# Kernel optimization log

Measured on AMD Instinct MI355X. Metric: run time of the kernel, lower is better.

The kernel has to match this reference:

```python
import jax, jax.numpy as jnp
import numpy as np

B, C_IN, C_OUT, H, W, K, NK = 16, 256, 256, 64, 64, 3, 2
EPS = 1e-8


def setup_inputs() -> dict:
    key = jax.random.key(0)
    k1, k2, k3, k4 = jax.random.split(key, 4)
    x = jax.random.normal(k1, (B, C_IN, H, W), dtype=jnp.float32)
    mod = jax.random.normal(k2, (B, C_IN), dtype=jnp.float32)
    kernel_mod = jax.random.normal(k3, (B, NK), dtype=jnp.float32)
    # kernel bank: [num_conv_kernels, dim_out, dim_in, k, k] (kaiming-ish scale)
    weights = jax.random.normal(k4, (NK, C_OUT, C_IN, K, K), dtype=jnp.float32) / np.sqrt(C_IN * K * K)
    gamma = jnp.ones((C_OUT,), dtype=jnp.float32)
    return {"x": x, "mod": mod, "kernel_mod": kernel_mod, "weights": weights, "gamma": gamma}


def _block(x, mod, kernel_mod, weights, gamma):
    # adaptive kernel selection: softmax-mix the kernel bank per sample
    attn = jax.nn.softmax(kernel_mod, axis=-1)                       # [b, n]
    w = jnp.einsum('bn,noikl->boikl', attn, weights)                 # [b, o, i, k, k]
    # style modulation over input channels
    w = w * (mod[:, None, :, None, None] + 1.0)
    # demodulation
    denom = jnp.clip(jnp.sum(w * w, axis=(2, 3, 4), keepdims=True), EPS)
    w = w * jax.lax.rsqrt(denom)
    # per-sample conv (groups=b trick in torch) -> vmap over batch
    def conv_one(fmap, wb):
        return jax.lax.conv_general_dilated(
            fmap[None], wb, window_strides=(1, 1), padding='SAME',
            dimension_numbers=('NCHW', 'OIHW', 'NCHW'))[0]
    y = jax.vmap(conv_one)(x, w)                                     # [b, o, h, w]
    # RMSNorm over channel dim: F.normalize(x, dim=1) * gamma * sqrt(dim)
    norm = jnp.sqrt(jnp.sum(y * y, axis=1, keepdims=True))
    y = y / jnp.maximum(norm, 1e-12)
    y = y * gamma[None, :, None, None] * (gamma.shape[0] ** 0.5)
    # SiLU
    return y * jax.nn.sigmoid(y)


def reference(x, mod, kernel_mod, weights, gamma):
    return _block(x, mod, kernel_mod, weights, gamma)
```

## Files before the change

### kernel.cpp

```cpp
#include <hip/hip_runtime.h>
#include <math.h>


typedef __attribute__((ext_vector_type(8))) short short8;
typedef __attribute__((ext_vector_type(4))) float f32x4;

#define GLL16(src, dst)                                                       \
  __builtin_amdgcn_global_load_lds(                                           \
      (const __attribute__((address_space(1))) unsigned int*)(src),           \
      (__attribute__((address_space(3))) unsigned int*)(dst), 16, 0, 0)

static __device__ __forceinline__ unsigned short f2bf(float v) {
  union { float f; unsigned u; } u;
  u.f = v;
  unsigned r = u.u + 0x7FFF + ((u.u >> 16) & 1);
  return (unsigned short)(r >> 16);
}

__global__ __launch_bounds__(256) void scale_kernel(
    const float* __restrict__ mod, const float* __restrict__ kmod,
    const float* __restrict__ weights, float* __restrict__ scale) {
  int bo = blockIdx.x;
  int b = bo >> 8, o = bo & 255;

  float k0 = kmod[b * 2 + 0], k1 = kmod[b * 2 + 1];
  float mx = fmaxf(k0, k1);
  float e0 = expf(k0 - mx), e1 = expf(k1 - mx);
  float ai = 1.0f / (e0 + e1);
  float a0 = e0 * ai, a1 = e1 * ai;

  int t = threadIdx.x;
  const float* w0 = weights + (size_t)o * 2304;
  const float* w1 = w0 + 589824;

  float s = 0.0f;
#pragma unroll
  for (int r = 0; r < 9; r++) {
    int idx = t + r * 256;
    int i = idx / 9;
    float wv = a0 * w0[idx] + a1 * w1[idx];
    wv *= (mod[b * 256 + i] + 1.0f);
    s += wv * wv;
  }
#pragma unroll
  for (int off = 32; off > 0; off >>= 1) s += __shfl_down(s, off);

  __shared__ float red[4];
  if ((t & 63) == 0) red[t >> 6] = s;
  __syncthreads();
  if (t == 0) {
    float tot = red[0] + red[1] + red[2] + red[3];
    scale[bo] = rsqrtf(fmaxf(tot, 1e-8f));
  }
}

__global__ __launch_bounds__(256) void wprep(
    const float* __restrict__ mod, const float* __restrict__ kmod,
    const float* __restrict__ weights, const float* __restrict__ scale,
    unsigned short* __restrict__ wq) {
  __shared__ __align__(16) unsigned short buf[10240];
  int blk = blockIdx.x;
  int b = blk >> 6, ot = (blk >> 4) & 3, c = blk & 15;
  int t = threadIdx.x;

  float k0 = kmod[b * 2 + 0], k1 = kmod[b * 2 + 1];
  float mx = fmaxf(k0, k1);
  float e0 = expf(k0 - mx), e1 = expf(k1 - mx);
  float ai = 1.0f / (e0 + e1);
  float a0 = e0 * ai, a1 = e1 * ai;

#pragma unroll
  for (int k = 0; k < 4; ++k) {
    int e = t + k * 256;
    int half = e >> 9;
    buf[(half * 10 + 9) * 512 + (e & 511)] = 0;
  }

  int ol = t >> 2, q = t & 3;
  int o = ot * 64 + ol;
  float sc = scale[b * 256 + o];
#pragma unroll
  for (int io = 0; io < 2; ++io) {
#pragma unroll
    for (int e2 = 0; e2 < 2; ++e2) {
      int e = q * 2 + e2;
      int i = c * 16 + io * 8 + e;
      float f = (mod[b * 256 + i] + 1.0f) * sc;
      const float* w0 = &weights[((size_t)o * 256 + i) * 9];
      const float* w1 = w0 + 589824;
#pragma unroll
      for (int j = 0; j < 9; ++j) {
        float v = (a0 * w0[j] + a1 * w1[j]) * f;
        buf[(io * 10 + j) * 512 + ol * 8 + e] = f2bf(v);
      }
    }
  }
  __syncthreads();
  size_t base = (size_t)blk * 10240;
#pragma unroll
  for (int k = 0; k < 5; ++k) {
    int idx = t + k * 256;
    *(short8*)(wq + base + (size_t)idx * 8) = *(const short8*)&buf[idx * 8];
  }
}

__global__ __launch_bounds__(256) void xprep(
    const float* __restrict__ x, unsigned short* __restrict__ xq) {
  int blk = blockIdx.x;
  int rowp = blk % 66;
  int bc = blk / 66;
  int b = bc >> 4, c = bc & 15;
  int t = threadIdx.x;
  size_t obase = (size_t)blk * 1056;

  if (rowp == 0 || rowp == 65) {
    for (int idx = t; idx < 1056; idx += 256) xq[obase + idx] = 0;
    return;
  }
  __shared__ __align__(16) unsigned short xs2[1056];
  int row = rowp - 1;
  for (int idx = t; idx < 1056; idx += 256) xs2[idx] = 0;
  __syncthreads();
#pragma unroll
  for (int k = 0; k < 4; ++k) {
    int idx = t + k * 256;
    int il = idx >> 6, col = idx & 63;
    float v = x[(((size_t)b * 256 + c * 16 + il) * 64 + row) * 64 + col];
    xs2[(col + 1) * 16 + il] = f2bf(v);
  }
  __syncthreads();
  if (t < 132) *(short8*)(xq + obase + (size_t)t * 8) = *(const short8*)&xs2[t * 8];
}

__global__ __launch_bounds__(256, 2) void conv_mfma(
    const unsigned short* __restrict__ xq, const unsigned short* __restrict__ wq,
    float* __restrict__ out) {
  __shared__ __align__(16) unsigned short wsm[2][10240];
  __shared__ __align__(16) unsigned short xsm[2][9504];

  int bid = blockIdx.x;
  int xcd = bid & 7;
  int kk = bid >> 3;
  int b = xcd * 2 + (kk >> 6);
  int rem = kk & 63;
  int ot = rem >> 4;
  int rt = rem & 15;
  int r0 = rt * 4;

  int t = threadIdx.x;
  int w = t >> 6, lane = t & 63;
  int g = (t >> 4) & 3, lm = t & 15;

  int baddr_[5], aaddr_[5];
#pragma unroll
  for (int s = 0; s < 5; ++s) {
    int p = 4 * s + g;
    int io = (p >= 10) ? 1 : 0;
    int j = p - 10 * io;
    int jd3, jm3;
    if (j == 9) { jd3 = 0; jm3 = 0; }
    else { jd3 = (j >= 3) + (j >= 6); jm3 = j - 3 * jd3; }
    baddr_[s] = ((w + jd3) * 66 + lm + jm3) * 48 + io * 16;
    aaddr_[s] = p * 1024 + lm * 16;
  }

  int xo0, xo1, xo2, xo3;
  {
    int idx, rl, rm;
    idx = t;        rl = idx / 132; rm = idx - rl * 132; xo0 = (rl * 66 + (rm >> 1)) * 24 + (rm & 1) * 8;
    idx = t + 256;  rl = idx / 132; rm = idx - rl * 132; xo1 = (rl * 66 + (rm >> 1)) * 24 + (rm & 1) * 8;
    idx = t + 512;  rl = idx / 132; rm = idx - rl * 132; xo2 = (rl * 66 + (rm >> 1)) * 24 + (rm & 1) * 8;
    idx = t + 768;  rl = idx / 132; rm = idx - rl * 132; xo3 = (rl * 66 + (rm >> 1)) * 24 + (rm & 1) * 8;
  }

  f32x4 acc[4][4];
#pragma unroll
  for (int mf = 0; mf < 4; ++mf)
#pragma unroll
    for (int nf = 0; nf < 4; ++nf) acc[mf][nf] = (f32x4){0.f, 0.f, 0.f, 0.f};

  short8 xr0, xr1, xr2, xr3;

#define XLOAD(cn)                                                              \
  {                                                                            \
    const unsigned short* xs_ =                                                \
        xq + (size_t)((b * 16 + (cn)) * 66 + r0) * 1056;                       \
    xr0 = *(const short8*)(xs_ + (size_t)t * 8);                               \
    xr1 = *(const short8*)(xs_ + (size_t)(t + 256) * 8);                       \
    xr2 = *(const short8*)(xs_ + (size_t)(t + 512) * 8);                       \
    if (t < 24) xr3 = *(const short8*)(xs_ + (size_t)(t + 768) * 8);           \
  }

#define WSTAGE(cn, nb)                                                         \
  {                                                                            \
    const unsigned short* ws_ =                                                \
        wq + ((size_t)(b * 4 + ot) * 16 + (cn)) * 10240 + w * 2560 + lane * 8; \
    unsigned short* wd_ = &wsm[nb][w * 2560];                                  \
    _Pragma("unroll")                                                          \
    for (int it = 0; it < 5; ++it) GLL16(ws_ + it * 512, wd_ + it * 512);      \
  }

#define XWRITE(nb)                                                             \
  {                                                                            \
    *(short8*)&xsm[nb][xo0] = xr0;                                             \
    *(short8*)&xsm[nb][xo1] = xr1;                                             \
    *(short8*)&xsm[nb][xo2] = xr2;                                             \
    if (t < 24) *(short8*)&xsm[nb][xo3] = xr3;                                 \
  }

  XLOAD(0);
  WSTAGE(0, 0);
  XWRITE(0);
  __syncthreads();

  for (int c = 0; c < 16; ++c) {
    int cur = c & 1;
    if (c < 15) {
      XLOAD(c + 1);
      WSTAGE(c + 1, cur ^ 1);
    }
    {
      const char* wsb = (const char*)wsm[cur];
      const char* xsb = (const char*)xsm[cur];
#pragma unroll
      for (int s = 0; s < 5; ++s) {
        short8 A[4];
#pragma unroll
        for (int mf = 0; mf < 4; ++mf)
          A[mf] = *(const short8*)(wsb + aaddr_[s] + mf * 256);
#pragma unroll
        for (int nf = 0; nf < 4; ++nf) {
          short8 Bf = *(const short8*)(xsb + baddr_[s] + nf * 768);
#pragma unroll
          for (int mf = 0; mf < 4; ++mf)
            acc[mf][nf] =
                __builtin_amdgcn_mfma_f32_16x16x32_bf16(A[mf], Bf, acc[mf][nf], 0, 0, 0);
        }
      }
    }
    if (c < 15) XWRITE(cur ^ 1);
    __syncthreads();
  }

  int row = r0 + w;
#pragma unroll
  for (int mf = 0; mf < 4; ++mf)
#pragma unroll
    for (int nf = 0; nf < 4; ++nf)
#pragma unroll
      for (int q = 0; q < 4; ++q) {
        int o = ot * 64 + mf * 16 + g * 4 + q;
        int col = nf * 16 + lm;
        out[(((size_t)b * 256 + o) * 64 + row) * 64 + col] = acc[mf][nf][q];
      }
#undef XLOAD
#undef WSTAGE
#undef XWRITE
}

__global__ __launch_bounds__(256) void norm_kernel(
    float* __restrict__ y, const float* __restrict__ gamma) {
  int blk = blockIdx.x;
  int b = blk >> 6, h = blk & 63;
  int t = threadIdx.x;
  int p = t & 63, og = t >> 6;

  size_t base = (((size_t)b * 256) * 64 + h) * 64 + p;
  float yv[64];
  float s = 0.0f;
#pragma unroll
  for (int k = 0; k < 64; k++) {
    yv[k] = y[base + (size_t)(og * 64 + k) * 4096];
    s = fmaf(yv[k], yv[k], s);
  }

  __shared__ float red[4][64];
  __shared__ float invs[64];
  red[og][p] = s;
  __syncthreads();
  if (og == 0) {
    float tot = red[0][p] + red[1][p] + red[2][p] + red[3][p];
    float nrm = sqrtf(tot);
    invs[p] = 16.0f / fmaxf(nrm, 1e-12f);
  }
  __syncthreads();
  float iv = invs[p];
#pragma unroll
  for (int k = 0; k < 64; k++) {
    int o = og * 64 + k;
    float v = yv[k] * iv * gamma[o];
    float sg = 1.0f / (1.0f + expf(-v));
    y[base + (size_t)o * 4096] = v * sg;
  }
}

extern "C" void kernel_launch(void* const* d_in, const int* in_sizes, int n_in,
                              void* d_out, int out_size, void* d_ws, size_t ws_size,
                              hipStream_t stream) {
  const float* x = (const float*)d_in[0];
  const float* mod = (const float*)d_in[1];
  const float* kmod = (const float*)d_in[2];
  const float* weights = (const float*)d_in[3];
  const float* gamma = (const float*)d_in[4];
  float* out = (float*)d_out;

  unsigned short* wq = (unsigned short*)d_ws;
  float* scale = (float*)((char*)d_ws + 20971520);
  unsigned short* xq = (unsigned short*)((char*)d_ws + 20987904);

  scale_kernel<<<16 * 256, 256, 0, stream>>>(mod, kmod, weights, scale);
  wprep<<<1024, 256, 0, stream>>>(mod, kmod, weights, scale, wq);
  xprep<<<16 * 16 * 66, 256, 0, stream>>>(x, xq);
  conv_mfma<<<1024, 256, 0, stream>>>(xq, wq, out);
  norm_kernel<<<16 * 64, 256, 0, stream>>>(out, gamma);
}
```

Measured before the change: 139.4 us.

## Shrink conv LDS footprint with XOR-swizzled x tile and single weight buffer for 3 blocks/CU

The weight tile now goes through registers into a single LDS buffer instead of double-buffered global_load_lds. The x tile drops from a padded 48-byte stride to a dense 32-byte stride with an XOR swizzle to avoid bank conflicts. Together these cut shared memory per block so launch bounds can request three blocks per CU instead of two, aiming to hide latency with more occupancy. The cost is an extra barrier per channel step, since the single weight buffer must be drained before it is overwritten, plus more registers held for the prefetched weights.

```diff
diff --git a/kernel.cpp b/kernel.cpp
--- a/kernel.cpp
+++ b/kernel.cpp
@@ -4,11 +4,6 @@
 
 typedef __attribute__((ext_vector_type(8))) short short8;
 typedef __attribute__((ext_vector_type(4))) float f32x4;
-
-#define GLL16(src, dst)                                                       \
-  __builtin_amdgcn_global_load_lds(                                           \
-      (const __attribute__((address_space(1))) unsigned int*)(src),           \
-      (__attribute__((address_space(3))) unsigned int*)(dst), 16, 0, 0)
 
 static __device__ __forceinline__ unsigned short f2bf(float v) {
   union { float f; unsigned u; } u;
@@ -132,11 +127,11 @@
   if (t < 132) *(short8*)(xq + obase + (size_t)t * 8) = *(const short8*)&xs2[t * 8];
 }
 
-__global__ __launch_bounds__(256, 2) void conv_mfma(
+__global__ __launch_bounds__(256, 3) void conv_mfma(
     const unsigned short* __restrict__ xq, const unsigned short* __restrict__ wq,
     float* __restrict__ out) {
-  __shared__ __align__(16) unsigned short wsm[2][10240];
-  __shared__ __align__(16) unsigned short xsm[2][9504];
+  __shared__ __align__(16) unsigned short wsm[10240];
+  __shared__ __align__(16) unsigned short xsm[2][6336];
 
   int bid = blockIdx.x;
   int xcd = bid & 7;
@@ -160,19 +155,12 @@
     int jd3, jm3;
     if (j == 9) { jd3 = 0; jm3 = 0; }
     else { jd3 = (j >= 3) + (j >= 6); jm3 = j - 3 * jd3; }
-    baddr_[s] = ((w + jd3) * 66 + lm + jm3) * 48 + io * 16;
+    int ba = ((w + jd3) * 66 + lm + jm3) * 32 + io * 16;
+    ba ^= ((ba >> 7) & 1) << 4;
+    baddr_[s] = ba;
     aaddr_[s] = p * 1024 + lm * 16;
   }
 
-  int xo0, xo1, xo2, xo3;
-  {
-    int idx, rl, rm;
-    idx = t;        rl = idx / 132; rm = idx - rl * 132; xo0 = (rl * 66 + (rm >> 1)) * 24 + (rm & 1) * 8;
-    idx = t + 256;  rl = idx / 132; rm = idx - rl * 132; xo1 = (rl * 66 + (rm >> 1)) * 24 + (rm & 1) * 8;
-    idx = t + 512;  rl = idx / 132; rm = idx - rl * 132; xo2 = (rl * 66 + (rm >> 1)) * 24 + (rm & 1) * 8;
-    idx = t + 768;  rl = idx / 132; rm = idx - rl * 132; xo3 = (rl * 66 + (rm >> 1)) * 24 + (rm & 1) * 8;
-  }
-
   f32x4 acc[4][4];
 #pragma unroll
   for (int mf = 0; mf < 4; ++mf)
@@ -180,6 +168,12 @@
     for (int nf = 0; nf < 4; ++nf) acc[mf][nf] = (f32x4){0.f, 0.f, 0.f, 0.f};
 
   short8 xr0, xr1, xr2, xr3;
+  short8 wr0, wr1, wr2, wr3, wr4;
+
+  int xw0 = (t * 16) ^ (((t * 16 >> 7) & 1) << 4);
+  int xw1 = ((t + 256) * 16) ^ ((((t + 256) * 16 >> 7) & 1) << 4);
+  int xw2 = ((t + 512) * 16) ^ ((((t + 512) * 16 >> 7) & 1) << 4);
+  int xw3 = ((t + 768) * 16) ^ ((((t + 768) * 16 >> 7) & 1) << 4);
 
 #define XLOAD(cn)                                                              \
   {                                                                            \
@@ -191,36 +185,50 @@
     if (t < 24) xr3 = *(const short8*)(xs_ + (size_t)(t + 768) * 8);           \
   }
 
-#define WSTAGE(cn, nb)                                                         \
+#define WLOAD(cn)                                                              \
   {                                                                            \
     const unsigned short* ws_ =                                                \
-        wq + ((size_t)(b * 4 + ot) * 16 + (cn)) * 10240 + w * 2560 + lane * 8; \
-    unsigned short* wd_ = &wsm[nb][w * 2560];                                  \
-    _Pragma("unroll")                                                          \
-    for (int it = 0; it < 5; ++it) GLL16(ws_ + it * 512, wd_ + it * 512);      \
+        wq + ((size_t)(b * 4 + ot) * 16 + (cn)) * 10240 + t * 8;               \
+    wr0 = *(const short8*)(ws_ + 0 * 2048);                                    \
+    wr1 = *(const short8*)(ws_ + 1 * 2048);                                    \
+    wr2 = *(const short8*)(ws_ + 2 * 2048);                                    \
+    wr3 = *(const short8*)(ws_ + 3 * 2048);                                    \
+    wr4 = *(const short8*)(ws_ + 4 * 2048);                                    \
   }
 
 #define XWRITE(nb)                                                             \
   {                                                                            \
-    *(short8*)&xsm[nb][xo0] = xr0;                                             \
-    *(short8*)&xsm[nb][xo1] = xr1;                                             \
-    *(short8*)&xsm[nb][xo2] = xr2;                                             \
-    if (t < 24) *(short8*)&xsm[nb][xo3] = xr3;                                 \
+    char* xb_ = (char*)xsm[nb];                                                \
+    *(short8*)(xb_ + xw0) = xr0;                                               \
+    *(short8*)(xb_ + xw1) = xr1;                                               \
+    *(short8*)(xb_ + xw2) = xr2;                                               \
+    if (t < 24) *(short8*)(xb_ + xw3) = xr3;                                   \
+  }
+
+#define WWRITE()                                                               \
+  {                                                                            \
+    short8* wb_ = (short8*)wsm;                                                \
+    wb_[t + 0 * 256] = wr0;                                                    \
+    wb_[t + 1 * 256] = wr1;                                                    \
+    wb_[t + 2 * 256] = wr2;                                                    \
+    wb_[t + 3 * 256] = wr3;                                                    \
+    wb_[t + 4 * 256] = wr4;                                                    \
   }
 
   XLOAD(0);
-  WSTAGE(0, 0);
+  WLOAD(0);
   XWRITE(0);
+  WWRITE();
   __syncthreads();
 
   for (int c = 0; c < 16; ++c) {
     int cur = c & 1;
     if (c < 15) {
       XLOAD(c + 1);
-      WSTAGE(c + 1, cur ^ 1);
+      WLOAD(c + 1);
     }
     {
-      const char* wsb = (const char*)wsm[cur];
+      const char* wsb = (const char*)wsm;
       const char* xsb = (const char*)xsm[cur];
 #pragma unroll
       for (int s = 0; s < 5; ++s) {
@@ -230,7 +238,7 @@
           A[mf] = *(const short8*)(wsb + aaddr_[s] + mf * 256);
 #pragma unroll
         for (int nf = 0; nf < 4; ++nf) {
-          short8 Bf = *(const short8*)(xsb + baddr_[s] + nf * 768);
+          short8 Bf = *(const short8*)(xsb + baddr_[s] + nf * 512);
 #pragma unroll
           for (int mf = 0; mf < 4; ++mf)
             acc[mf][nf] =
@@ -238,8 +246,12 @@
         }
       }
     }
-    if (c < 15) XWRITE(cur ^ 1);
     __syncthreads();
+    if (c < 15) {
+      XWRITE(cur ^ 1);
+      WWRITE();
+      __syncthreads();
+    }
   }
 
   int row = r0 + w;
@@ -254,8 +266,9 @@
         out[(((size_t)b * 256 + o) * 64 + row) * 64 + col] = acc[mf][nf][q];
       }
 #undef XLOAD
-#undef WSTAGE
+#undef WLOAD
 #undef XWRITE
+#undef WWRITE
 }
 
 __global__ __launch_bounds__(256) void norm_kernel(
```

After: 140.1 us. Within noise of the previous version (+0.5%).
